# Kernel optimization log

Measured on AMD Instinct MI355X. Metric: run time of the kernel, lower is better.

Reference implementation:

```python
import jax, jax.numpy as jnp
import numpy as np

T, B, D, H = 256, 2048, 16, 64


def _init_cell(key, in_dim, hidden):
    k1, k2, k3, k4 = jax.random.split(key, 4)
    s = 1.0 / np.sqrt(hidden)
    return (
        jax.random.uniform(k1, (4 * hidden, in_dim), minval=-s, maxval=s),
        jax.random.uniform(k2, (4 * hidden, hidden), minval=-s, maxval=s),
        jax.random.uniform(k3, (4 * hidden,), minval=-s, maxval=s),
        jax.random.uniform(k4, (4 * hidden,), minval=-s, maxval=s),
    )


def setup_inputs() -> dict:
    key = jax.random.key(0)
    kx, k0, k1, k2 = jax.random.split(key, 4)
    x = jax.random.normal(kx, (T, B, D), dtype=jnp.float32)
    W_ih0, W_hh0, b_ih0, b_hh0 = _init_cell(k0, D, H)
    W_ih1, W_hh1, b_ih1, b_hh1 = _init_cell(k1, H, H)
    W_ih2, W_hh2, b_ih2, b_hh2 = _init_cell(k2, H, H)
    return dict(x=x,
                W_ih0=W_ih0, W_hh0=W_hh0, b_ih0=b_ih0, b_hh0=b_hh0,
                W_ih1=W_ih1, W_hh1=W_hh1, b_ih1=b_ih1, b_hh1=b_hh1,
                W_ih2=W_ih2, W_hh2=W_hh2, b_ih2=b_ih2, b_hh2=b_hh2)


def _lstm_cell(x_t, h, c, W_ih, W_hh, b_ih, b_hh):
    # torch.nn.LSTMCell gate order: i, f, g, o
    gates = x_t @ W_ih.T + b_ih + h @ W_hh.T + b_hh  # (B, 4H)
    i, f, g, o = jnp.split(gates, 4, axis=-1)
    c_new = jax.nn.sigmoid(f) * c + jax.nn.sigmoid(i) * jnp.tanh(g)
    h_new = jax.nn.sigmoid(o) * jnp.tanh(c_new)
    return h_new, c_new


def reference(x, W_ih0, W_hh0, b_ih0, b_hh0,
              W_ih1, W_hh1, b_ih1, b_hh1,
              W_ih2, W_hh2, b_ih2, b_hh2):
    Bsz = x.shape[1]
    z = jnp.zeros((Bsz, H), dtype=x.dtype)
    init = (z, z, z, z, z, z)  # h0,h1,h2,c0,c1,c2

    def step(state, x_t):
        h0, h1, h2, c0, c1, c2 = state
        h0, c0 = _lstm_cell(x_t, h0, c0, W_ih0, W_hh0, b_ih0, b_hh0)
        h1, c1 = _lstm_cell(h0, h1, c1, W_ih1, W_hh1, b_ih1, b_hh1)
        h2, c2 = _lstm_cell(h1, h2, c2, W_ih2, W_hh2, b_ih2, b_hh2)
        return (h0, h1, h2, c0, c1, c2), h2

    _, out = jax.lax.scan(step, init, x)  # out: (T, B, H)
    return out
```

## Files before the change

### kernel.cpp

```cpp
#include <hip/hip_runtime.h>
#include <hip/hip_bf16.h>


#define TT 256
#define BB 2048
#define DD 16
#define HH 64

#define SROW 216
#define PANEL (8 * SROW)
#define H0O 0
#define H1O 64
#define H2O 128
#define XO  192

#define L2E  1.4426950408889634f
#define L2E2 2.8853900817779268f

typedef __attribute__((ext_vector_type(8))) _Float16 halfx8;
typedef __attribute__((ext_vector_type(8))) unsigned short ushortx8;
typedef __attribute__((ext_vector_type(4))) float floatx4;

#if __has_builtin(__builtin_amdgcn_exp2f)
#define EXP2F(x) __builtin_amdgcn_exp2f(x)
#else
#define EXP2F(x) exp2f(x)
#endif
#if __has_builtin(__builtin_amdgcn_rcpf)
#define RCPF(x) __builtin_amdgcn_rcpf(x)
#else
#define RCPF(x) (1.0f/(x))
#endif

__device__ __forceinline__ float sigm_s(float xs) {
  return RCPF(1.0f + EXP2F(-xs));
}
__device__ __forceinline__ float tanh_s(float xs) {
  return 1.0f - 2.0f * RCPF(EXP2F(xs) + 1.0f);
}
__device__ __forceinline__ void block_sync() {
  asm volatile("s_waitcnt lgkmcnt(0)" ::: "memory");
  __builtin_amdgcn_s_barrier();
}

__device__ __forceinline__ halfx8 dpp_xor8(halfx8 v) {
  union { halfx8 h; int i[4]; } u, d;
  u.h = v;
#pragma unroll
  for (int k = 0; k < 4; ++k)
    d.i[k] = __builtin_amdgcn_update_dpp(0, u.i[k], 0x128, 0xf, 0xf, true);
  return d.h;
}

__global__ void detect_k(const unsigned short* __restrict__ xr, int* __restrict__ flag) {
  int cnt = 0;
  for (int i = threadIdx.x; i < 4096; i += 64) {
    float v = __uint_as_float(((unsigned int)xr[i]) << 16);
    if (!(fabsf(v) < 4.0f)) cnt++;
  }
#pragma unroll
  for (int o = 32; o > 0; o >>= 1) cnt += __shfl_down(cnt, o, 64);
  if (threadIdx.x == 0) flag[0] = (cnt < 100) ? 1 : 0;
}

#define MF(A, B, C) __builtin_amdgcn_mfma_f32_16x16x32_f16(A, B, C, 0, 0, 0)

#define BODY(S_, PPB, PNB)                                                        \
  {                                                                               \
    const int s_ = (S_);                                                          \
    halfx8 xreg = {};                                                             \
    const bool loader = (tid < 16) && (s_ + 1 < TT);                              \
    if (loader)                                                                   \
      xreg = ld8(xg, ((long)(s_ + 1) * BB + rowbase + (tid >> 1)) * DD + (tid & 1) * 8); \
    block_sync();                                                                 \
    const _Float16* PpR = SH + (PPB) + rd_offP;                                   \
    _Float16* Pn = SH + (PNB);                                                    \
    halfx8 pA = *(const halfx8*)(PpR + 0);                \
    halfx8 pB = *(const halfx8*)(PpR + 64);                               \
    halfx8 pC = *(const halfx8*)(PpR + 128);                              \
    halfx8 rX = *(const halfx8*)(SH + (PPB) + rd_offX);         \
    halfx8 sA = dpp_xor8(pA);                                                     \
    halfx8 sB = dpp_xor8(pB);                                                     \
    halfx8 sC = dpp_xor8(pC);                                                     \
    halfx8 r0 = m8 ? sA : pA, r1 = m8 ? pA : sA;                                  \
    halfx8 r2 = m8 ? sB : pB, r3 = m8 ? pB : sB;                                  \
    halfx8 r4 = m8 ? sC : pC, r5 = m8 ? pC : sC;                                  \
    floatx4 a0 = bs0, a1 = bs1, a2 = bs2;                                         \
    __builtin_amdgcn_s_setprio(1);                                                \
    a0 = MF(wA0[0], r0, a0); a2 = MF(wA2[0], r2, a2);                             \
    a0 = MF(wA0[1], r1, a0); a2 = MF(wA2[1], r3, a2);                             \
    a2 = MF(wA2[2], r4, a2); a0 = MF(wA0[2], rX, a0);                             \
    a2 = MF(wA2[3], r5, a2);                                                      \
    a1 = MF(wA1[0], r0, a1); a1 = MF(wA1[1], r1, a1);                             \
    a1 = MF(wA1[2], r2, a1); a1 = MF(wA1[3], r3, a1);                             \
    __builtin_amdgcn_s_setprio(0);                                                \
    {                       \
      floatx4 gv;                                                                 \
      gv[0] = m8 ? a2[0] : a0[0]; gv[1] = m8 ? a2[1] : a0[1];                     \
      gv[2] = m8 ? a2[2] : a0[2]; gv[3] = m8 ? a2[3] : a0[3];                     \
      float I = sigm_s(gv[0]), F = sigm_s(gv[1]);                                 \
      float G = tanh_s(gv[2]), O = sigm_s(gv[3]);                                 \
      float cn = F * cA + I * G;                                                  \
      float hn = O * tanh_s(L2E2 * cn);                                           \
      bool vA = m8 ? (s_ >= 2) : (s_ < TT);                                       \
      if (vA) {                                                                   \
        cA = cn; Pn[wrA] = (_Float16)hn;                                          \
        if (m8) {                                                                 \
          long oi = (long)(s_ - 2) * ((long)BB * HH) + olane;                     \
          if (isbf) ((__hip_bfloat16*)outp)[oi] = __float2bfloat16(hn);           \
          else ((float*)outp)[oi] = hn;                                           \
        }                                                                         \
      }                                                                           \
    }                                                                             \
    {                                            \
      float I = sigm_s(a1[0]), F = sigm_s(a1[1]);                                 \
      float G = tanh_s(a1[2]), O = sigm_s(a1[3]);                                 \
      float cn = F * cB + I * G;                                                  \
      float hn = O * tanh_s(L2E2 * cn);                                           \
      if (!m8 && s_ >= 1 && s_ <= TT) { cB = cn; Pn[wrB] = (_Float16)hn; }        \
    }                                                                             \
    if (loader) *(halfx8*)&Pn[(tid >> 1) * SROW + XO + (tid & 1) * 8] = xreg;     \
  }

__launch_bounds__(1024, 1)
__global__ void lstm3_k(const void* __restrict__ xg,
                        const void* W0i, const void* W0h, const void* B0i, const void* B0h,
                        const void* W1i, const void* W1h, const void* B1i, const void* B1h,
                        const void* W2i, const void* W2h, const void* B2i, const void* B2h,
                        void* __restrict__ outp, const int* __restrict__ flagp) {
  const int tid = threadIdx.x;
  const int W = tid >> 6;
  const int lane = tid & 63;
  const int c = lane & 15;
  const int g = lane >> 4;
  const int rowbase = blockIdx.x * 8;
  const int isbf = flagp ? flagp[0] : 1;

  __shared__ __align__(16) _Float16 SH[2 * PANEL + 32];

  auto ldf = [&](const void* b, long i) -> float {
    return isbf ? __bfloat162float(((const __hip_bfloat16*)b)[i]) : ((const float*)b)[i];
  };
  auto ld8 = [&](const void* b, long i) -> halfx8 {
    halfx8 r;
    if (isbf) {
      ushortx8 raw = *(const ushortx8*)((const unsigned short*)b + i);
#pragma unroll
      for (int j = 0; j < 8; ++j)
        r[j] = (_Float16)__uint_as_float(((unsigned int)raw[j]) << 16);
    } else {
      const float* s = (const float*)b + i;
#pragma unroll
      for (int j = 0; j < 8; ++j) r[j] = (_Float16)s[j];
    }
    return r;
  };
  auto ld8s = [&](const void* b, long i, float sc) -> halfx8 {
    halfx8 r;
    if (isbf) {
      ushortx8 raw = *(const ushortx8*)((const unsigned short*)b + i);
#pragma unroll
      for (int j = 0; j < 8; ++j)
        r[j] = (_Float16)(sc * __uint_as_float(((unsigned int)raw[j]) << 16));
    } else {
      const float* s = (const float*)b + i;
#pragma unroll
      for (int j = 0; j < 8; ++j) r[j] = (_Float16)(sc * s[j]);
    }
    return r;
  };

  halfx8 wA0[3], wA1[4], wA2[4];
  floatx4 bs0, bs1, bs2;
  {
    const int ril = W * 16 + c;
    const int u = ril >> 2, q = ril & 3;
    const long orig = q * 64 + u;
    const float sc = (q == 2) ? L2E2 : L2E;
    halfx8 z = {};
    wA0[0] = ld8s(W0h, orig * 64 + 8 * g, sc);
    wA0[1] = ld8s(W0h, orig * 64 + 32 + 8 * g, sc);
    wA0[2] = (g == 0) ? ld8s(W0i, orig * 16, sc)
           : (g == 1) ? ld8s(W0i, orig * 16 + 8, sc) : z;
    wA1[0] = ld8s(W1i, orig * 64 + 8 * g, sc);
    wA1[1] = ld8s(W1i, orig * 64 + 32 + 8 * g, sc);
    wA1[2] = ld8s(W1h, orig * 64 + 8 * g, sc);
    wA1[3] = ld8s(W1h, orig * 64 + 32 + 8 * g, sc);
    wA2[0] = ld8s(W2i, orig * 64 + 8 * g, sc);
    wA2[1] = ld8s(W2i, orig * 64 + 32 + 8 * g, sc);
    wA2[2] = ld8s(W2h, orig * 64 + 8 * g, sc);
    wA2[3] = ld8s(W2h, orig * 64 + 32 + 8 * g, sc);
    const int ub = 4 * W + g;
#pragma unroll
    for (int qq = 0; qq < 4; ++qq) {
      const float bsc = (qq == 2) ? L2E2 : L2E;
      bs0[qq] = bsc * (ldf(B0i, 64 * qq + ub) + ldf(B0h, 64 * qq + ub));
      bs1[qq] = bsc * (ldf(B1i, 64 * qq + ub) + ldf(B1h, 64 * qq + ub));
      bs2[qq] = bsc * (ldf(B2i, 64 * qq + ub) + ldf(B2h, 64 * qq + ub));
    }
  }

  for (int i = tid; i < 2 * PANEL + 32; i += 1024) SH[i] = (_Float16)0.0f;
  block_sync();
  if (tid < 16) {
    *(halfx8*)&SH[(tid >> 1) * SROW + XO + (tid & 1) * 8] =
        ld8(xg, ((long)0 * BB + rowbase + (tid >> 1)) * DD + (tid & 1) * 8);
  }

  const bool m8 = (c >= 8);
  const int r_el = c & 7;
  const int u_el = 4 * W + g;
  const int rd_offP = r_el * SROW + 8 * g + (m8 ? 32 : 0);
  const int rd_offX = r_el * SROW + 8 * g + XO;
  const int wrA = r_el * SROW + u_el + (m8 ? H2O : H0O);
  const int wrB = r_el * SROW + u_el + H1O;
  const long olane = ((long)rowbase + r_el) * HH + u_el;
  float cA = 0.f, cB = 0.f;

#pragma unroll 1
  for (int s2 = 0; s2 < (TT + 2) / 2; ++s2) {
    const int s = 2 * s2;
    BODY(s, 0, PANEL)
    BODY(s + 1, PANEL, 0)
  }
}

extern "C" void kernel_launch(void* const* d_in, const int* in_sizes, int n_in,
                              void* d_out, int out_size, void* d_ws, size_t ws_size,
                              hipStream_t stream) {
  (void)in_sizes; (void)n_in; (void)out_size;
  int* flag = (ws_size >= sizeof(int)) ? (int*)d_ws : nullptr;
  if (flag) {
    detect_k<<<dim3(1), dim3(64), 0, stream>>>((const unsigned short*)d_in[0], flag);
  }
  lstm3_k<<<dim3(BB / 8), dim3(1024), 0, stream>>>(
      d_in[0],
      d_in[1], d_in[2], d_in[3], d_in[4],
      d_in[5], d_in[6], d_in[7], d_in[8],
      d_in[9], d_in[10], d_in[11], d_in[12],
      d_out, flag);
}
```

Before: 309.1 us.

## Peel LSTM wavefront edges, drop DPP swaps, and share reciprocals in gate math

Splits the time loop into guarded prologue/epilogue steps and a guard-free steady-state body that uses incrementing pointers for output and x loads. The shared-memory row is widened so each lane reads all seven fp16 operand vectors directly from LDS instead of doing three DPP cross-lane swaps plus selects. The gate nonlinearities are merged so pairs of sigmoids/tanh share a single reciprocal, cutting transcendental ops. This costs more LDS reads per step and slightly different rounding from the product-of-denominators reciprocal.

```diff
diff --git a/kernel.cpp b/kernel.cpp
--- a/kernel.cpp
+++ b/kernel.cpp
@@ -7,7 +7,7 @@
 #define DD 16
 #define HH 64
 
-#define SROW 216
+#define SROW 232
 #define PANEL (8 * SROW)
 #define H0O 0
 #define H1O 64
@@ -32,24 +32,22 @@
 #define RCPF(x) (1.0f/(x))
 #endif
 
-__device__ __forceinline__ float sigm_s(float xs) {
-  return RCPF(1.0f + EXP2F(-xs));
-}
-__device__ __forceinline__ float tanh_s(float xs) {
-  return 1.0f - 2.0f * RCPF(EXP2F(xs) + 1.0f);
-}
+__device__ __forceinline__ float lstm_cell(const floatx4 gv, float& cSt) {
+  float Ei = EXP2F(-gv[0]), Ef = EXP2F(-gv[1]);
+  float Eg = EXP2F(gv[2]),  Eo = EXP2F(-gv[3]);
+  float Ai = 1.0f + Ei, Bf = 1.0f + Ef, Cg = 1.0f + Eg, Do = 1.0f + Eo;
+  float r1 = RCPF(Ai * Cg), r2 = RCPF(Bf * Do);
+  float I = r1 * Cg, G = 1.0f - 2.0f * (r1 * Ai);
+  float F = r2 * Do, O = r2 * Bf;
+  float cn = F * cSt + I * G;
+  cSt = cn;
+  float Fc = 1.0f + EXP2F(L2E2 * cn);
+  return O * (1.0f - 2.0f * RCPF(Fc));
+}
+
 __device__ __forceinline__ void block_sync() {
   asm volatile("s_waitcnt lgkmcnt(0)" ::: "memory");
   __builtin_amdgcn_s_barrier();
-}
-
-__device__ __forceinline__ halfx8 dpp_xor8(halfx8 v) {
-  union { halfx8 h; int i[4]; } u, d;
-  u.h = v;
-#pragma unroll
-  for (int k = 0; k < 4; ++k)
-    d.i[k] = __builtin_amdgcn_update_dpp(0, u.i[k], 0x128, 0xf, 0xf, true);
-  return d.h;
 }
 
 __global__ void detect_k(const unsigned short* __restrict__ xr, int* __restrict__ flag) {
@@ -65,7 +63,26 @@
 
 #define MF(A, B, C) __builtin_amdgcn_mfma_f32_16x16x32_f16(A, B, C, 0, 0, 0)
 
-#define BODY(S_, PPB, PNB)                                                        \
+#define READS_MFMA(PPB)                                                           \
+    const _Float16* PpR = SH + (PPB) + rd_off;                                    \
+    halfx8 r0 = *(const halfx8*)(PpR + 0);                                        \
+    halfx8 r1 = *(const halfx8*)(PpR + 32);                                       \
+    halfx8 r2 = *(const halfx8*)(PpR + 64);                                       \
+    halfx8 r3 = *(const halfx8*)(PpR + 96);                                      \
+    halfx8 r4 = *(const halfx8*)(PpR + 128);                                      \
+    halfx8 r5 = *(const halfx8*)(PpR + 160);                                      \
+    halfx8 r6 = *(const halfx8*)(PpR + 192);                                      \
+    floatx4 a0 = bs0, a1 = bs1, a2 = bs2;                                         \
+    __builtin_amdgcn_s_setprio(1);                                                \
+    a0 = MF(wA0[0], r0, a0); a2 = MF(wA2[0], r2, a2);                             \
+    a0 = MF(wA0[1], r1, a0); a2 = MF(wA2[1], r3, a2);                             \
+    a2 = MF(wA2[2], r4, a2); a0 = MF(wA0[2], r6, a0);                             \
+    a2 = MF(wA2[3], r5, a2);                                                      \
+    a1 = MF(wA1[0], r0, a1); a1 = MF(wA1[1], r1, a1);                             \
+    a1 = MF(wA1[2], r2, a1); a1 = MF(wA1[3], r3, a1);                             \
+    __builtin_amdgcn_s_setprio(0);
+
+#define BODY_G(S_, PPB, PNB)                                                      \
   {                                                                               \
     const int s_ = (S_);                                                          \
     halfx8 xreg = {};                                                             \
@@ -73,38 +90,16 @@
     if (loader)                                                                   \
       xreg = ld8(xg, ((long)(s_ + 1) * BB + rowbase + (tid >> 1)) * DD + (tid & 1) * 8); \
     block_sync();                                                                 \
-    const _Float16* PpR = SH + (PPB) + rd_offP;                                   \
+    READS_MFMA(PPB)                                                               \
     _Float16* Pn = SH + (PNB);                                                    \
-    halfx8 pA = *(const halfx8*)(PpR + 0);                \
-    halfx8 pB = *(const halfx8*)(PpR + 64);                               \
-    halfx8 pC = *(const halfx8*)(PpR + 128);                              \
-    halfx8 rX = *(const halfx8*)(SH + (PPB) + rd_offX);         \
-    halfx8 sA = dpp_xor8(pA);                                                     \
-    halfx8 sB = dpp_xor8(pB);                                                     \
-    halfx8 sC = dpp_xor8(pC);                                                     \
-    halfx8 r0 = m8 ? sA : pA, r1 = m8 ? pA : sA;                                  \
-    halfx8 r2 = m8 ? sB : pB, r3 = m8 ? pB : sB;                                  \
-    halfx8 r4 = m8 ? sC : pC, r5 = m8 ? pC : sC;                                  \
-    floatx4 a0 = bs0, a1 = bs1, a2 = bs2;                                         \
-    __builtin_amdgcn_s_setprio(1);                                                \
-    a0 = MF(wA0[0], r0, a0); a2 = MF(wA2[0], r2, a2);                             \
-    a0 = MF(wA0[1], r1, a0); a2 = MF(wA2[1], r3, a2);                             \
-    a2 = MF(wA2[2], r4, a2); a0 = MF(wA0[2], rX, a0);                             \
-    a2 = MF(wA2[3], r5, a2);                                                      \
-    a1 = MF(wA1[0], r0, a1); a1 = MF(wA1[1], r1, a1);                             \
-    a1 = MF(wA1[2], r2, a1); a1 = MF(wA1[3], r3, a1);                             \
-    __builtin_amdgcn_s_setprio(0);                                                \
-    {                       \
-      floatx4 gv;                                                                 \
+    { floatx4 gv;                                                                 \
       gv[0] = m8 ? a2[0] : a0[0]; gv[1] = m8 ? a2[1] : a0[1];                     \
       gv[2] = m8 ? a2[2] : a0[2]; gv[3] = m8 ? a2[3] : a0[3];                     \
-      float I = sigm_s(gv[0]), F = sigm_s(gv[1]);                                 \
-      float G = tanh_s(gv[2]), O = sigm_s(gv[3]);                                 \
-      float cn = F * cA + I * G;                                                  \
-      float hn = O * tanh_s(L2E2 * cn);                                           \
+      float ct = cA;                                                              \
+      float hn = lstm_cell(gv, ct);                                               \
       bool vA = m8 ? (s_ >= 2) : (s_ < TT);                                       \
       if (vA) {                                                                   \
-        cA = cn; Pn[wrA] = (_Float16)hn;                                          \
+        cA = ct; Pn[wrA] = (_Float16)hn;                                          \
         if (m8) {                                                                 \
           long oi = (long)(s_ - 2) * ((long)BB * HH) + olane;                     \
           if (isbf) ((__hip_bfloat16*)outp)[oi] = __float2bfloat16(hn);           \
@@ -112,14 +107,37 @@
         }                                                                         \
       }                                                                           \
     }                                                                             \
-    {                                            \
-      float I = sigm_s(a1[0]), F = sigm_s(a1[1]);                                 \
-      float G = tanh_s(a1[2]), O = sigm_s(a1[3]);                                 \
-      float cn = F * cB + I * G;                                                  \
-      float hn = O * tanh_s(L2E2 * cn);                                           \
-      if (!m8 && s_ >= 1 && s_ <= TT) { cB = cn; Pn[wrB] = (_Float16)hn; }        \
-    }                                                                             \
-    if (loader) *(halfx8*)&Pn[(tid >> 1) * SROW + XO + (tid & 1) * 8] = xreg;     \
+    { float ct = cB;                                                              \
+      float hn = lstm_cell(a1, ct);                                               \
+      if (s_ >= 1 && s_ <= TT) { cB = ct; Pn[wrB] = (_Float16)hn; }               \
+    }                                                                             \
+    if (loader) *(halfx8*)&Pn[xwr] = xreg;                                        \
+  }
+
+#define BODY_F(PPB, PNB)                                                          \
+  {                                                                               \
+    halfx8 xreg = {};                                                             \
+    const bool loader = (tid < 16);                                               \
+    if (loader) xreg = ld8(xg, xbase + xlane);                                    \
+    block_sync();                                                                 \
+    READS_MFMA(PPB)                                                               \
+    _Float16* Pn = SH + (PNB);                                                    \
+    { floatx4 gv;                                                                 \
+      gv[0] = m8 ? a2[0] : a0[0]; gv[1] = m8 ? a2[1] : a0[1];                     \
+      gv[2] = m8 ? a2[2] : a0[2]; gv[3] = m8 ? a2[3] : a0[3];                     \
+      float hn = lstm_cell(gv, cA);                                               \
+      Pn[wrA] = (_Float16)hn;                                                     \
+      if (m8) {                                                                   \
+        if (isbf) *(__hip_bfloat16*)op = __float2bfloat16(hn);                    \
+        else      *(float*)op = hn;                                               \
+      }                                                                           \
+    }                                                                             \
+    op += ostep;                                                                  \
+    { float hn = lstm_cell(a1, cB);                                               \
+      Pn[wrB] = (_Float16)hn;             \
+    }                                                                             \
+    if (loader) *(halfx8*)&Pn[xwr] = xreg;                                        \
+    xbase += (long)BB * DD;                                                       \
   }
 
 __launch_bounds__(1024, 1)
@@ -210,19 +228,28 @@
   const bool m8 = (c >= 8);
   const int r_el = c & 7;
   const int u_el = 4 * W + g;
-  const int rd_offP = r_el * SROW + 8 * g + (m8 ? 32 : 0);
-  const int rd_offX = r_el * SROW + 8 * g + XO;
+  const int rd_off = r_el * SROW + 8 * g;
   const int wrA = r_el * SROW + u_el + (m8 ? H2O : H0O);
   const int wrB = r_el * SROW + u_el + H1O;
+  const int xwr = (tid >> 1) * SROW + XO + (tid & 1) * 8;
+  const int xlane = (rowbase + (tid >> 1)) * DD + (tid & 1) * 8;
   const long olane = ((long)rowbase + r_el) * HH + u_el;
+  const long ostep = (long)BB * HH * (isbf ? 2 : 4);
+  char* op = (char*)outp + (isbf ? 2 : 4) * olane;
   float cA = 0.f, cB = 0.f;
-
+  long xbase = (long)3 * BB * DD;
+
+  BODY_G(0, 0, PANEL)
+  BODY_G(1, PANEL, 0)
 #pragma unroll 1
-  for (int s2 = 0; s2 < (TT + 2) / 2; ++s2) {
-    const int s = 2 * s2;
-    BODY(s, 0, PANEL)
-    BODY(s + 1, PANEL, 0)
-  }
+  for (int s2 = 1; s2 < 127; ++s2) {
+    BODY_F(0, PANEL)
+    BODY_F(PANEL, 0)
+  }
+  BODY_G(254, 0, PANEL)
+  BODY_G(255, PANEL, 0)
+  BODY_G(256, 0, PANEL)
+  BODY_G(257, PANEL, 0)
 }
 
 extern "C" void kernel_launch(void* const* d_in, const int* in_sizes, int n_in,
```

New measurement: 274.3 us. -11.3%, faster.
